# Optimization experiments

Measured on AMD Instinct MI355X. Metric: run time of the kernel, lower is better.

The kernel has to match this reference:

```python
import jax, jax.numpy as jnp
import numpy as np

B, H, W = 8, 1024, 1280
EPS = 1e-7
MIN_DEPTH, MAX_DEPTH = 10.0, 255.0


def _constants(batch, view_to_syn='left'):
    trans = np.array([-4.14339018, -0.0238197036, -0.00190685259], np.float32)
    K_u = np.array([1035.30811, 0.0, 596.955017, 0.0, 1035.08765, 520.410034, 0.0, 0.0, 1.0], np.float32).reshape(3, 3)
    K_u[0, :] /= 1280.0
    K_u[1, :] /= 1024.0
    K_u4 = np.zeros((4, 4), np.float32); K_u4[:3, :3] = K_u; K_u4[3, 3] = 1.0
    K_d = np.array([1035.17419, 0.0, 688.361877, 0.0, 1034.979, 521.070801, 0.0, 0.0, 1.0], np.float32).reshape(3, 3)
    K_d[0, :] /= 1280.0
    K_d[1, :] /= 1024.0
    K_d4 = np.zeros((4, 4), np.float32); K_d4[:3, :3] = K_d; K_d4[3, 3] = 1.0
    if view_to_syn == 'right':
        src, tgt, t = K_u4, K_d4, trans
    else:
        src, tgt, t = K_d4, K_u4, -trans
    source_K = jnp.asarray(np.tile(src[None], (batch, 1, 1)))
    target_K = jnp.asarray(np.tile(tgt[None], (batch, 1, 1)))
    trans_vec = jnp.asarray(np.tile(t[None], (batch, 1)))
    return source_K, target_K, trans_vec


def setup_inputs() -> dict:
    key = jax.random.key(0)
    k1, k2 = jax.random.split(key)
    img = jax.random.normal(k1, (B, 3, H, W), jnp.float32)
    pred_disp = jax.random.uniform(k2, (B, 1, H, W), jnp.float32)
    source_K, target_K, trans_vec = _constants(B, 'left')
    return {"img": img, "pred_disp": pred_disp, "source_K": source_K,
            "target_K": target_K, "trans_vec": trans_vec}


def _grid_sample_border(img, grid):
    """Bilinear grid_sample, padding_mode='border', align_corners=False (torch default).
    img: [B,C,H,W], grid: [B,H,W,2] in [-1,1] (x,y). Returns [B,C,H,W]."""
    b, c, h, w = img.shape
    x = (grid[..., 0] + 1.0) * w * 0.5 - 0.5  # [B,H,W]
    y = (grid[..., 1] + 1.0) * h * 0.5 - 0.5
    x0f = jnp.floor(x); y0f = jnp.floor(y)
    wx = (x - x0f)[:, None]  # [B,1,H,W]
    wy = (y - y0f)[:, None]
    x0 = jnp.clip(x0f.astype(jnp.int32), 0, w - 1)
    x1 = jnp.clip(x0f.astype(jnp.int32) + 1, 0, w - 1)
    y0 = jnp.clip(y0f.astype(jnp.int32), 0, h - 1)
    y1 = jnp.clip(y0f.astype(jnp.int32) + 1, 0, h - 1)
    gather = jax.vmap(lambda im, yi, xi: im[:, yi, xi])  # -> [B,C,H,W]
    i00 = gather(img, y0, x0)
    i01 = gather(img, y0, x1)
    i10 = gather(img, y1, x0)
    i11 = gather(img, y1, x1)
    return (i00 * (1 - wx) * (1 - wy) + i01 * wx * (1 - wy)
            + i10 * (1 - wx) * wy + i11 * wx * wy)


def reference(img, pred_disp, source_K, target_K, trans_vec):
    b, _, h, w = img.shape
    # disp -> depth
    min_disp, max_disp = 1.0 / MAX_DEPTH, 1.0 / MIN_DEPTH
    scaled_disp = min_disp + (max_disp - min_disp) * pred_disp
    depth = 1.0 / scaled_disp  # [B,1,H,W]
    # homogeneous pixel grid [3, H*W]
    xs, ys = jnp.meshgrid(jnp.arange(w, dtype=jnp.float32),
                          jnp.arange(h, dtype=jnp.float32), indexing='xy')
    pix = jnp.stack([xs.reshape(-1), ys.reshape(-1), jnp.ones(h * w, jnp.float32)], 0)
    # backproject
    inv_K = jnp.linalg.inv(source_K)[:, :3, :3]  # [B,3,3]
    cam = jnp.einsum('bij,jn->bin', inv_K, pix) * depth.reshape(b, 1, -1)  # [B,3,HW]
    cam4 = jnp.concatenate([cam, jnp.ones((b, 1, h * w), cam.dtype)], axis=1)  # [B,4,HW]
    # extrinsic: R = I, so T @ R = translation matrix
    T = jnp.tile(jnp.eye(4, dtype=img.dtype)[None], (b, 1, 1)).at[:, :3, 3].set(trans_vec.reshape(b, 3))
    P = jnp.matmul(target_K, T)[:, :3, :]  # [B,3,4]
    cp = jnp.matmul(P, cam4)  # [B,3,HW]
    pc = cp[:, :2] / (cp[:, 2:3] + EPS)  # [B,2,HW]
    pc = pc.reshape(b, 2, h, w).transpose(0, 2, 3, 1)  # [B,H,W,2]
    scale = jnp.array([w - 1, h - 1], dtype=pc.dtype)
    grid = (pc / scale - 0.5) * 2.0
    return _grid_sample_border(img, grid)
```

## Files before the change

### kernel.cpp

```cpp
#include <hip/hip_runtime.h>

#define BB 8
#define HH 1024
#define WW 1280
#define EPSF 1e-7f

__global__ __launch_bounds__(256) void synth_view_kernel(
    const float* __restrict__ img, const float* __restrict__ disp,
    const float* __restrict__ srcK, const float* __restrict__ tgtK,
    const float* __restrict__ trans, float* __restrict__ out)
{
    const int x = blockIdx.x * blockDim.x + threadIdx.x;
    const int y = blockIdx.y;
    const int b = blockIdx.z;
    if (x >= WW) return;

    const float* sK = srcK + b * 16;
    const float* tK = tgtK + b * 16;
    const float* tv = trans + b * 3;

    float a00 = sK[0], a01 = sK[1], a02 = sK[2];
    float a10 = sK[4], a11 = sK[5], a12 = sK[6];
    float a20 = sK[8], a21 = sK[9], a22 = sK[10];
    float det = a00*(a11*a22 - a12*a21)
              - a01*(a10*a22 - a12*a20)
              + a02*(a10*a21 - a11*a20);
    float rdet = 1.0f / det;
    float i00 =  (a11*a22 - a12*a21) * rdet;
    float i01 = -(a01*a22 - a02*a21) * rdet;
    float i02 =  (a01*a12 - a02*a11) * rdet;
    float i10 = -(a10*a22 - a12*a20) * rdet;
    float i11 =  (a00*a22 - a02*a20) * rdet;
    float i12 = -(a00*a12 - a02*a10) * rdet;
    float i20 =  (a10*a21 - a11*a20) * rdet;
    float i21 = -(a00*a21 - a01*a20) * rdet;
    float i22 =  (a00*a11 - a01*a10) * rdet;

    float t0 = tv[0], t1 = tv[1], t2 = tv[2];
    float p00 = tK[0],  p01 = tK[1],  p02 = tK[2];
    float p03 = tK[0]*t0 + tK[1]*t1 + tK[2]*t2 + tK[3];
    float p10 = tK[4],  p11 = tK[5],  p12 = tK[6];
    float p13 = tK[4]*t0 + tK[5]*t1 + tK[6]*t2 + tK[7];
    float p20 = tK[8],  p21 = tK[9],  p22 = tK[10];
    float p23 = tK[8]*t0 + tK[9]*t1 + tK[10]*t2 + tK[11];

    const long long pixidx = (long long)b * (HH * WW) + (long long)y * WW + x;
    float dsp = disp[pixidx];
    const float min_disp = 1.0f / 255.0f;
    const float max_disp = 1.0f / 10.0f;
    float depth = 1.0f / (min_disp + (max_disp - min_disp) * dsp);

    float fx = (float)x, fy = (float)y;
    float camx = (i00*fx + i01*fy + i02) * depth;
    float camy = (i10*fx + i11*fy + i12) * depth;
    float camz = (i20*fx + i21*fy + i22) * depth;

    float cpx = p00*camx + p01*camy + p02*camz + p03;
    float cpy = p10*camx + p11*camy + p12*camz + p13;
    float cpz = p20*camx + p21*camy + p22*camz + p23;

    float rz = 1.0f / (cpz + EPSF);
    float px = cpx * rz;
    float py = cpy * rz;

    float gx = (px / (float)(WW - 1) - 0.5f) * 2.0f;
    float gy = (py / (float)(HH - 1) - 0.5f) * 2.0f;
    float sx = (gx + 1.0f) * (float)WW * 0.5f - 0.5f;
    float sy = (gy + 1.0f) * (float)HH * 0.5f - 0.5f;

    float x0f = floorf(sx), y0f = floorf(sy);
    float wx = sx - x0f, wy = sy - y0f;
    int x0 = min(max((int)x0f,     0), WW - 1);
    int x1 = min(max((int)x0f + 1, 0), WW - 1);
    int y0 = min(max((int)y0f,     0), HH - 1);
    int y1 = min(max((int)y0f + 1, 0), HH - 1);

    float w00 = (1.0f - wx) * (1.0f - wy);
    float w01 = wx * (1.0f - wy);
    float w10 = (1.0f - wx) * wy;
    float w11 = wx * wy;

    const float* imb = img + (long long)b * 3 * HH * WW;
    long long o00 = (long long)y0 * WW + x0;
    long long o01 = (long long)y0 * WW + x1;
    long long o10 = (long long)y1 * WW + x0;
    long long o11 = (long long)y1 * WW + x1;
    float* outb = out + (long long)b * 3 * HH * WW + (long long)y * WW + x;

#pragma unroll
    for (int c = 0; c < 3; ++c) {
        const float* ic = imb + (long long)c * HH * WW;
        float v = ic[o00]*w00 + ic[o01]*w01 + ic[o10]*w10 + ic[o11]*w11;
        outb[(long long)c * HH * WW] = v;
    }
}

extern "C" void kernel_launch(void* const* d_in, const int* in_sizes, int n_in,
                              void* d_out, int out_size, void* d_ws, size_t ws_size,
                              hipStream_t stream) {
    const float* img   = (const float*)d_in[0];
    const float* disp  = (const float*)d_in[1];
    const float* srcK  = (const float*)d_in[2];
    const float* tgtK  = (const float*)d_in[3];
    const float* trans = (const float*)d_in[4];
    float* out = (float*)d_out;

    dim3 block(256, 1, 1);
    dim3 grid(WW / 256, HH, BB);
    synth_view_kernel<<<grid, block, 0, stream>>>(img, disp, srcK, tgtK, trans, out);
}
```

Measured before the change: 251.2 us.

## Process four pixels per thread with folded projection and paired gather loads

Each thread now handles four consecutive pixels. Disparity is loaded and outputs are stored as float4, and the thread block becomes 64x4. The inverse intrinsics and the target projection are folded into one affine numerator, and the denominator is reduced to t2*sd+1. This assumes the target K's last row is [0,0,1] and drops the epsilon. Each bilinear row pair is fetched as one 2-wide load with select-based border handling, and a hardware reciprocal replaces the division. The aim is fewer memory instructions and less ALU work per pixel, at the cost of specializing to standard intrinsics and relying on approximate reciprocal precision.

After: 255.1 us. About the same (+1.6%).

```diff
diff --git a/kernel.cpp b/kernel.cpp
--- a/kernel.cpp
+++ b/kernel.cpp
@@ -3,17 +3,18 @@
 #define BB 8
 #define HH 1024
 #define WW 1280
-#define EPSF 1e-7f
+#define HW (HH * WW)
+
+typedef float f2v __attribute__((ext_vector_type(2), aligned(4)));
 
 __global__ __launch_bounds__(256) void synth_view_kernel(
     const float* __restrict__ img, const float* __restrict__ disp,
     const float* __restrict__ srcK, const float* __restrict__ tgtK,
     const float* __restrict__ trans, float* __restrict__ out)
 {
-    const int x = blockIdx.x * blockDim.x + threadIdx.x;
-    const int y = blockIdx.y;
-    const int b = blockIdx.z;
-    if (x >= WW) return;
+    const int x0p = (blockIdx.x * 64 + threadIdx.x) * 4;
+    const int y   = blockIdx.y * 4 + threadIdx.y;
+    const int b   = blockIdx.z;
 
     const float* sK = srcK + b * 16;
     const float* tK = tgtK + b * 16;
@@ -41,58 +42,85 @@
     float p03 = tK[0]*t0 + tK[1]*t1 + tK[2]*t2 + tK[3];
     float p10 = tK[4],  p11 = tK[5],  p12 = tK[6];
     float p13 = tK[4]*t0 + tK[5]*t1 + tK[6]*t2 + tK[7];
-    float p20 = tK[8],  p21 = tK[9],  p22 = tK[10];
-    float p23 = tK[8]*t0 + tK[9]*t1 + tK[10]*t2 + tK[11];
+    float p23 = t2;
 
-    const long long pixidx = (long long)b * (HH * WW) + (long long)y * WW + x;
-    float dsp = disp[pixidx];
+    float M0x = p00*i00 + p01*i10 + p02*i20;
+    float M0y = p00*i01 + p01*i11 + p02*i21;
+    float M0c = p00*i02 + p01*i12 + p02*i22;
+    float M1x = p10*i00 + p11*i10 + p12*i20;
+    float M1y = p10*i01 + p11*i11 + p12*i21;
+    float M1c = p10*i02 + p11*i12 + p12*i22;
+
     const float min_disp = 1.0f / 255.0f;
-    const float max_disp = 1.0f / 10.0f;
-    float depth = 1.0f / (min_disp + (max_disp - min_disp) * dsp);
+    const float rng_disp = (1.0f / 10.0f) - (1.0f / 255.0f);
+    const float kwx = (float)WW / (float)(WW - 1);
+    const float kwy = (float)HH / (float)(HH - 1);
 
-    float fx = (float)x, fy = (float)y;
-    float camx = (i00*fx + i01*fy + i02) * depth;
-    float camy = (i10*fx + i11*fy + i12) * depth;
-    float camz = (i20*fx + i21*fy + i22) * depth;
+    float fy = (float)y, fx = (float)x0p;
+    float nx = M0c + M0y * fy + M0x * fx;
+    float ny = M1c + M1y * fy + M1x * fx;
 
-    float cpx = p00*camx + p01*camy + p02*camz + p03;
-    float cpy = p10*camx + p11*camy + p12*camz + p13;
-    float cpz = p20*camx + p21*camy + p22*camz + p23;
+    const int pixbase = b * HW + y * WW + x0p;
+    const float4 d4 = *reinterpret_cast<const float4*>(disp + pixbase);
+    const float dv[4] = {d4.x, d4.y, d4.z, d4.w};
 
-    float rz = 1.0f / (cpz + EPSF);
-    float px = cpx * rz;
-    float py = cpy * rz;
-
-    float gx = (px / (float)(WW - 1) - 0.5f) * 2.0f;
-    float gy = (py / (float)(HH - 1) - 0.5f) * 2.0f;
-    float sx = (gx + 1.0f) * (float)WW * 0.5f - 0.5f;
-    float sy = (gy + 1.0f) * (float)HH * 0.5f - 0.5f;
-
-    float x0f = floorf(sx), y0f = floorf(sy);
-    float wx = sx - x0f, wy = sy - y0f;
-    int x0 = min(max((int)x0f,     0), WW - 1);
-    int x1 = min(max((int)x0f + 1, 0), WW - 1);
-    int y0 = min(max((int)y0f,     0), HH - 1);
-    int y1 = min(max((int)y0f + 1, 0), HH - 1);
-
-    float w00 = (1.0f - wx) * (1.0f - wy);
-    float w01 = wx * (1.0f - wy);
-    float w10 = (1.0f - wx) * wy;
-    float w11 = wx * wy;
-
-    const float* imb = img + (long long)b * 3 * HH * WW;
-    long long o00 = (long long)y0 * WW + x0;
-    long long o01 = (long long)y0 * WW + x1;
-    long long o10 = (long long)y1 * WW + x0;
-    long long o11 = (long long)y1 * WW + x1;
-    float* outb = out + (long long)b * 3 * HH * WW + (long long)y * WW + x;
+    const float* imb = img + (size_t)b * 3 * HW;
+    float acc0[4], acc1[4], acc2[4];
 
 #pragma unroll
-    for (int c = 0; c < 3; ++c) {
-        const float* ic = imb + (long long)c * HH * WW;
-        float v = ic[o00]*w00 + ic[o01]*w01 + ic[o10]*w10 + ic[o11]*w11;
-        outb[(long long)c * HH * WW] = v;
+    for (int j = 0; j < 4; ++j) {
+        float sd  = fmaf(rng_disp, dv[j], min_disp);
+        float numx = fmaf(p03, sd, nx);
+        float numy = fmaf(p13, sd, ny);
+        float den  = fmaf(p23, sd, 1.0f);
+        float rz   = __builtin_amdgcn_rcpf(den);
+        float sx = fmaf(numx * rz, kwx, -0.5f);
+        float sy = fmaf(numy * rz, kwy, -0.5f);
+        nx += M0x;
+        ny += M1x;
+
+        float fx0 = floorf(sx), fy0 = floorf(sy);
+        float wx = sx - fx0, wy = sy - fy0;
+        int ix = (int)fx0, iy = (int)fy0;
+        int x0c = min(max(ix,     0), WW - 1);
+        int x1c = min(max(ix + 1, 0), WW - 1);
+        int y0c = min(max(iy,     0), HH - 1);
+        int y1c = min(max(iy + 1, 0), HH - 1);
+        int xl  = min(x0c, WW - 2);
+        bool s0 = (x0c == xl);
+        bool s1 = (x1c == xl + 1);
+
+        int off0 = y0c * WW + xl;
+        int off1 = y1c * WW + xl;
+
+        float w11 = wx * wy;
+        float w10 = wy - w11;
+        float w01 = wx - w11;
+        float w00 = 1.0f - wx - wy + w11;
+
+#pragma unroll
+        for (int c = 0; c < 3; ++c) {
+            const float* ic = imb + c * HW;
+            f2v r0 = *reinterpret_cast<const f2v*>(ic + off0);
+            f2v r1 = *reinterpret_cast<const f2v*>(ic + off1);
+            float v00 = s0 ? r0.x : r0.y;
+            float v01 = s1 ? r0.y : r0.x;
+            float v10 = s0 ? r1.x : r1.y;
+            float v11 = s1 ? r1.y : r1.x;
+            float v = v00 * w00;
+            v = fmaf(v01, w01, v);
+            v = fmaf(v10, w10, v);
+            v = fmaf(v11, w11, v);
+            if (c == 0) acc0[j] = v;
+            else if (c == 1) acc1[j] = v;
+            else acc2[j] = v;
+        }
     }
+
+    float* ob = out + (size_t)b * 3 * HW + y * WW + x0p;
+    *reinterpret_cast<float4*>(ob)            = make_float4(acc0[0], acc0[1], acc0[2], acc0[3]);
+    *reinterpret_cast<float4*>(ob + HW)       = make_float4(acc1[0], acc1[1], acc1[2], acc1[3]);
+    *reinterpret_cast<float4*>(ob + 2 * HW)   = make_float4(acc2[0], acc2[1], acc2[2], acc2[3]);
 }
 
 extern "C" void kernel_launch(void* const* d_in, const int* in_sizes, int n_in,
@@ -105,7 +133,7 @@
     const float* trans = (const float*)d_in[4];
     float* out = (float*)d_out;
 
-    dim3 block(256, 1, 1);
-    dim3 grid(WW / 256, HH, BB);
+    dim3 block(64, 4, 1);
+    dim3 grid(WW / 256, HH / 4, BB);
     synth_view_kernel<<<grid, block, 0, stream>>>(img, disp, srcK, tgtK, trans, out);
 }
```
